# Kernel tuning notes

Measured on AMD Instinct MI355X. Metric: run time of the kernel, lower is better.

The kernel has to match this reference:

```python
import jax, jax.numpy as jnp
import numpy as np

B, C_IN, C_OUT, N = 4, 32, 32, 163842


def setup_inputs() -> dict:
    key = jax.random.key(0)
    k1, k2, k3, k4 = jax.random.split(key, 4)
    x = jax.random.normal(k1, (B, C_IN, N), dtype=jnp.float32)
    # nn.Linear(7*in_feats, out_feats): weight [out, 7*in], bias [out]
    W = jax.random.normal(k2, (C_OUT, 7 * C_IN), dtype=jnp.float32) * (1.0 / np.sqrt(7 * C_IN))
    b = jax.random.normal(k3, (C_OUT,), dtype=jnp.float32) * 0.01
    neigh_orders = jax.random.randint(k4, (N, 7), 0, N, dtype=jnp.int32)
    return {"x": x, "W": W, "b": b, "neigh_orders": neigh_orders}


def reference(x, W, b, neigh_orders):
    # x: [B, C_in, N] -> [B, N, C_in]
    xt = jnp.transpose(x, (0, 2, 1))
    # gather 1-ring neighborhood: [B, N, 7, C_in]
    gathered = xt[:, neigh_orders, :]
    Bb, Nn = xt.shape[0], xt.shape[1]
    mat = gathered.reshape(Bb, Nn, 7 * xt.shape[2])  # [B, N, 7*C_in]
    out = jnp.einsum("bnk,ok->bno", mat, W) + b       # [B, N, C_out]
    return jnp.transpose(out, (0, 2, 1))              # [B, C_out, N]
```

## Files before the change

### kernel.cpp

```cpp
#include <hip/hip_runtime.h>
#include <hip/hip_bf16.h>
#include <stdint.h>

#define B_   4
#define CIN  32
#define COUT 32
#define NV   163842
#define K7   7

typedef short bf16x8 __attribute__((ext_vector_type(8)));
typedef float f32x4  __attribute__((ext_vector_type(4)));

__device__ inline uint16_t f2bf(float f) {
    uint32_t u = __float_as_uint(f);
    uint32_t r = (u + 0x7FFFu + ((u >> 16) & 1u)) >> 16;
    return (uint16_t)r;
}

__global__ void k_convw(const float* __restrict__ W, uint16_t* __restrict__ Wb) {
    int i = blockIdx.x * 256 + threadIdx.x;
    if (i < COUT * K7 * CIN) Wb[i] = f2bf(W[i]);
}

__global__ void k_transpose(const float* __restrict__ x, uint16_t* __restrict__ xt) {
    int v = blockIdx.x * 256 + threadIdx.x;
    int b = blockIdx.y;
    if (v >= NV) return;
    const float* xb = x + (size_t)b * CIN * NV;
    uint16_t* row = xt + (size_t)v * (B_ * CIN) + b * CIN;
    #pragma unroll
    for (int q = 0; q < 4; ++q) {
        bf16x8 pk;
        #pragma unroll
        for (int i = 0; i < 8; ++i) {
            float f = xb[(size_t)(q * 8 + i) * NV + v];
            ((uint16_t*)&pk)[i] = f2bf(f);
        }
        *(bf16x8*)(row + q * 8) = pk;
    }
}

__global__ __launch_bounds__(256) void k_main(const uint16_t* __restrict__ xt,
                                              const uint16_t* __restrict__ Wb,
                                              const float* __restrict__ bias,
                                              const int* __restrict__ neigh,
                                              float* __restrict__ out) {
    const int tid  = threadIdx.x;
    const int lane = tid & 63;
    const int wv   = tid >> 6;
    const int vb   = blockIdx.x * 64 + wv * 16;
    const int l15  = lane & 15;
    const int g    = lane >> 4;
    const int v    = vb + l15;
    const int vv   = (v < NV) ? v : (NV - 1);

    bf16x8 wf[2][K7];
    #pragma unroll
    for (int t = 0; t < 2; ++t)
        #pragma unroll
        for (int j = 0; j < K7; ++j)
            wf[t][j] = *(const bf16x8*)(Wb + (size_t)(t * 16 + l15) * (K7 * CIN) + j * CIN + g * 8);

    int nidx[K7];
    #pragma unroll
    for (int j = 0; j < K7; ++j) nidx[j] = neigh[(size_t)vv * K7 + j];

    f32x4 acc[B_][2];
    #pragma unroll
    for (int b = 0; b < B_; ++b) {
        acc[b][0] = (f32x4){0.f, 0.f, 0.f, 0.f};
        acc[b][1] = (f32x4){0.f, 0.f, 0.f, 0.f};
    }

    #pragma unroll
    for (int j = 0; j < K7; ++j) {
        const uint16_t* row = xt + (size_t)nidx[j] * (B_ * CIN);
        bf16x8 xf[B_];
        #pragma unroll
        for (int b = 0; b < B_; ++b)
            xf[b] = *(const bf16x8*)(row + b * CIN + g * 8);
        #pragma unroll
        for (int b = 0; b < B_; ++b) {
            acc[b][0] = __builtin_amdgcn_mfma_f32_16x16x32_bf16(wf[0][j], xf[b], acc[b][0], 0, 0, 0);
            acc[b][1] = __builtin_amdgcn_mfma_f32_16x16x32_bf16(wf[1][j], xf[b], acc[b][1], 0, 0, 0);
        }
    }

    if (v < NV) {
        f32x4 bia0 = *(const f32x4*)(bias + g * 4);
        f32x4 bia1 = *(const f32x4*)(bias + 16 + g * 4);
        #pragma unroll
        for (int b = 0; b < B_; ++b) {
            float* ob = out + (size_t)b * COUT * NV + v;
            #pragma unroll
            for (int r = 0; r < 4; ++r) {
                int o0 = g * 4 + r;
                ob[(size_t)o0 * NV] = acc[b][0][r] + bia0[r];
                int o1 = 16 + g * 4 + r;
                ob[(size_t)o1 * NV] = acc[b][1][r] + bia1[r];
            }
        }
    }
}

extern "C" void kernel_launch(void* const* d_in, const int* in_sizes, int n_in,
                              void* d_out, int out_size, void* d_ws, size_t ws_size,
                              hipStream_t stream) {
    const float* x     = (const float*)d_in[0];
    const float* W     = (const float*)d_in[1];
    const float* bias  = (const float*)d_in[2];
    const int*   neigh = (const int*)d_in[3];
    float* out = (float*)d_out;

    uint16_t* xt = (uint16_t*)d_ws;
    uint16_t* Wb = xt + (size_t)NV * B_ * CIN;

    k_convw<<<(COUT * K7 * CIN + 255) / 256, 256, 0, stream>>>(W, Wb);

    dim3 g1((NV + 255) / 256, B_);
    k_transpose<<<g1, 256, 0, stream>>>(x, xt);

    dim3 g2((NV + 63) / 64, 1);
    k_main<<<g2, 256, 0, stream>>>(xt, Wb, bias, neigh, out);
}
```

Before: 244.2 us.

## Coalesce transpose stores via LDS and stage gathered rows through double-buffered LDS

The transpose kernel now packs 64 vertices across all batches into shared memory and then writes contiguous 16-byte chunks, so its global stores are coalesced instead of strided. The main kernel's gather is reorganised: each group of 4 lanes fetches one full 256-byte neighbour row with 16-byte loads. Those rows go into per-wave double-buffered LDS tiles with padding and are read back in MFMA operand layout, and the next neighbour's loads are issued early so they overlap with the current MFMAs. This costs extra LDS traffic and registers, and there is no explicit barrier between the intra-wave LDS writes and reads.

```diff
diff --git a/kernel.cpp b/kernel.cpp
--- a/kernel.cpp
+++ b/kernel.cpp
@@ -22,29 +22,50 @@
     if (i < COUT * K7 * CIN) Wb[i] = f2bf(W[i]);
 }
 
-__global__ void k_transpose(const float* __restrict__ x, uint16_t* __restrict__ xt) {
-    int v = blockIdx.x * 256 + threadIdx.x;
-    int b = blockIdx.y;
-    if (v >= NV) return;
-    const float* xb = x + (size_t)b * CIN * NV;
-    uint16_t* row = xt + (size_t)v * (B_ * CIN) + b * CIN;
+__global__ __launch_bounds__(256) void k_transpose(const float* __restrict__ x,
+                                                   uint16_t* __restrict__ xt) {
+    __shared__ uint16_t lds[64 * 132];
+    const int v0 = blockIdx.x * 64;
+    const int b  = threadIdx.x >> 6;
+    const int vl = threadIdx.x & 63;
+    const int v  = v0 + vl;
+
+    if (v < NV) {
+        const float* xb = x + (size_t)b * CIN * NV + v;
+        #pragma unroll
+        for (int q = 0; q < 4; ++q) {
+            bf16x8 pk;
+            #pragma unroll
+            for (int i = 0; i < 8; ++i)
+                ((uint16_t*)&pk)[i] = f2bf(xb[(size_t)(q * 8 + i) * NV]);
+            *(bf16x8*)&lds[vl * 132 + b * 32 + q * 8] = pk;
+        }
+    }
+    __syncthreads();
+
+    const size_t lim = ((size_t)(NV - v0)) * 256;
+    uint16_t* dst = xt + (size_t)v0 * 128;
+    const int tid = threadIdx.x;
     #pragma unroll
-    for (int q = 0; q < 4; ++q) {
-        bf16x8 pk;
-        #pragma unroll
-        for (int i = 0; i < 8; ++i) {
-            float f = xb[(size_t)(q * 8 + i) * NV + v];
-            ((uint16_t*)&pk)[i] = f2bf(f);
+    for (int s = 0; s < 4; ++s) {
+        const int f = s * 4096 + tid * 16;
+        if ((size_t)f < lim) {
+            const int row = f >> 8;
+            const int w   = f & 255;
+            bf16x8 d = *(bf16x8*)&lds[row * 132 + (w >> 1)];
+            *(bf16x8*)(dst + (f >> 1)) = d;
         }
-        *(bf16x8*)(row + q * 8) = pk;
     }
 }
+
+#define MFMA_BF16 __builtin_amdgcn_mfma_f32_16x16x32_bf16
 
 __global__ __launch_bounds__(256) void k_main(const uint16_t* __restrict__ xt,
                                               const uint16_t* __restrict__ Wb,
                                               const float* __restrict__ bias,
                                               const int* __restrict__ neigh,
                                               float* __restrict__ out) {
+    __shared__ uint16_t lds[4][2][16 * 132];
     const int tid  = threadIdx.x;
     const int lane = tid & 63;
     const int wv   = tid >> 6;
@@ -52,7 +73,10 @@
     const int l15  = lane & 15;
     const int g    = lane >> 4;
     const int v    = vb + l15;
-    const int vv   = (v < NV) ? v : (NV - 1);
+    const int gr   = lane >> 2;
+    const int gc   = lane & 3;
+    const int gv   = vb + gr;
+    const int gvv  = (gv < NV) ? gv : (NV - 1);
 
     bf16x8 wf[2][K7];
     #pragma unroll
@@ -61,9 +85,9 @@
         for (int j = 0; j < K7; ++j)
             wf[t][j] = *(const bf16x8*)(Wb + (size_t)(t * 16 + l15) * (K7 * CIN) + j * CIN + g * 8);
 
-    int nidx[K7];
+    int nidxg[K7];
     #pragma unroll
-    for (int j = 0; j < K7; ++j) nidx[j] = neigh[(size_t)vv * K7 + j];
+    for (int j = 0; j < K7; ++j) nidxg[j] = neigh[(size_t)gvv * K7 + j];
 
     f32x4 acc[B_][2];
     #pragma unroll
@@ -72,19 +96,42 @@
         acc[b][1] = (f32x4){0.f, 0.f, 0.f, 0.f};
     }
 
-    #pragma unroll
-    for (int j = 0; j < K7; ++j) {
-        const uint16_t* row = xt + (size_t)nidx[j] * (B_ * CIN);
-        bf16x8 xf[B_];
-        #pragma unroll
-        for (int b = 0; b < B_; ++b)
-            xf[b] = *(const bf16x8*)(row + b * CIN + g * 8);
-        #pragma unroll
-        for (int b = 0; b < B_; ++b) {
-            acc[b][0] = __builtin_amdgcn_mfma_f32_16x16x32_bf16(wf[0][j], xf[b], acc[b][0], 0, 0, 0);
-            acc[b][1] = __builtin_amdgcn_mfma_f32_16x16x32_bf16(wf[1][j], xf[b], acc[b][1], 0, 0, 0);
-        }
-    }
+    const char* xtb = (const char*)xt;
+    f32x4 ra0, ra1, ra2, ra3, rb0, rb1, rb2, rb3;
+
+#define ISSUE(R0, R1, R2, R3, j) { \
+    const char* _s = xtb + (size_t)nidxg[j] * 256 + gc * 16; \
+    R0 = *(const f32x4*)(_s);       R1 = *(const f32x4*)(_s + 64); \
+    R2 = *(const f32x4*)(_s + 128); R3 = *(const f32x4*)(_s + 192); }
+
+#define WRITE(R0, R1, R2, R3, BUF) { \
+    uint16_t* _d = &lds[wv][BUF][gr * 132 + gc * 8]; \
+    *(f32x4*)(_d)      = R0; *(f32x4*)(_d + 32) = R1; \
+    *(f32x4*)(_d + 64) = R2; *(f32x4*)(_d + 96) = R3; }
+
+#define RM(BUF, j) { \
+    const uint16_t* _r = &lds[wv][BUF][l15 * 132 + g * 8]; \
+    bf16x8 xf0 = *(const bf16x8*)(_r); \
+    bf16x8 xf1 = *(const bf16x8*)(_r + 32); \
+    bf16x8 xf2 = *(const bf16x8*)(_r + 64); \
+    bf16x8 xf3 = *(const bf16x8*)(_r + 96); \
+    acc[0][0] = MFMA_BF16(wf[0][j], xf0, acc[0][0], 0, 0, 0); \
+    acc[0][1] = MFMA_BF16(wf[1][j], xf0, acc[0][1], 0, 0, 0); \
+    acc[1][0] = MFMA_BF16(wf[0][j], xf1, acc[1][0], 0, 0, 0); \
+    acc[1][1] = MFMA_BF16(wf[1][j], xf1, acc[1][1], 0, 0, 0); \
+    acc[2][0] = MFMA_BF16(wf[0][j], xf2, acc[2][0], 0, 0, 0); \
+    acc[2][1] = MFMA_BF16(wf[1][j], xf2, acc[2][1], 0, 0, 0); \
+    acc[3][0] = MFMA_BF16(wf[0][j], xf3, acc[3][0], 0, 0, 0); \
+    acc[3][1] = MFMA_BF16(wf[1][j], xf3, acc[3][1], 0, 0, 0); }
+
+    ISSUE(ra0, ra1, ra2, ra3, 0);
+    ISSUE(rb0, rb1, rb2, rb3, 1); WRITE(ra0, ra1, ra2, ra3, 0); RM(0, 0);
+    ISSUE(ra0, ra1, ra2, ra3, 2); WRITE(rb0, rb1, rb2, rb3, 1); RM(1, 1);
+    ISSUE(rb0, rb1, rb2, rb3, 3); WRITE(ra0, ra1, ra2, ra3, 0); RM(0, 2);
+    ISSUE(ra0, ra1, ra2, ra3, 4); WRITE(rb0, rb1, rb2, rb3, 1); RM(1, 3);
+    ISSUE(rb0, rb1, rb2, rb3, 5); WRITE(ra0, ra1, ra2, ra3, 0); RM(0, 4);
+    ISSUE(ra0, ra1, ra2, ra3, 6); WRITE(rb0, rb1, rb2, rb3, 1); RM(1, 5);
+                                  WRITE(ra0, ra1, ra2, ra3, 0); RM(0, 6);
 
     if (v < NV) {
         f32x4 bia0 = *(const f32x4*)(bias + g * 4);
@@ -117,7 +164,7 @@
 
     k_convw<<<(COUT * K7 * CIN + 255) / 256, 256, 0, stream>>>(W, Wb);
 
-    dim3 g1((NV + 255) / 256, B_);
+    dim3 g1((NV + 63) / 64, 1);
     k_transpose<<<g1, 256, 0, stream>>>(x, xt);
 
     dim3 g2((NV + 63) / 64, 1);
```

Result: faster. 237.0 us (-2.9%).

## Stage transpose through LDS for coalesced writes and hoist all gathers in main

Applied to the files above, without the earlier changes.

The transpose kernel now handles 128 vertices across all batches per block, packs bf16 rows into padded shared memory, and writes the xt rows back as contiguous 16-byte chunks, so global stores are coalesced instead of strided by 256 bytes. In the main kernel, all 28 neighbor-row loads are issued before any MFMA, and launch bounds now request 2 blocks per CU, to get more memory-level parallelism. The cost is more registers held live for the prefetched fragments and 33 KB of LDS per transpose block.

```diff
diff --git a/kernel.cpp b/kernel.cpp
--- a/kernel.cpp
+++ b/kernel.cpp
@@ -22,29 +22,51 @@
     if (i < COUT * K7 * CIN) Wb[i] = f2bf(W[i]);
 }
 
-__global__ void k_transpose(const float* __restrict__ x, uint16_t* __restrict__ xt) {
-    int v = blockIdx.x * 256 + threadIdx.x;
-    int b = blockIdx.y;
-    if (v >= NV) return;
-    const float* xb = x + (size_t)b * CIN * NV;
-    uint16_t* row = xt + (size_t)v * (B_ * CIN) + b * CIN;
+__global__ __launch_bounds__(256) void k_transpose(const float* __restrict__ x,
+                                                   uint16_t* __restrict__ xt) {
+    __shared__ uint16_t lds[128 * 132];
+    const int v0 = blockIdx.x * 128;
+    const int t  = threadIdx.x;
+    const int vl = t & 127;
+    const int h  = t >> 7;
+    const int v  = v0 + vl;
+    const int vc = (v < NV) ? v : (NV - 1);
+
     #pragma unroll
-    for (int q = 0; q < 4; ++q) {
-        bf16x8 pk;
+    for (int b = 0; b < B_; ++b) {
+        const float* xb = x + (size_t)b * CIN * NV + (size_t)h * 16 * NV + vc;
         #pragma unroll
-        for (int i = 0; i < 8; ++i) {
-            float f = xb[(size_t)(q * 8 + i) * NV + v];
-            ((uint16_t*)&pk)[i] = f2bf(f);
+        for (int q = 0; q < 2; ++q) {
+            bf16x8 pk;
+            #pragma unroll
+            for (int i = 0; i < 8; ++i)
+                ((uint16_t*)&pk)[i] = f2bf(xb[(size_t)(q * 8 + i) * NV]);
+            *(bf16x8*)&lds[vl * 132 + b * 32 + h * 16 + q * 8] = pk;
         }
-        *(bf16x8*)(row + q * 8) = pk;
+    }
+    __syncthreads();
+
+    const size_t lim = ((size_t)(NV - v0)) * 256;
+    uint16_t* dst = xt + (size_t)v0 * 128;
+    #pragma unroll
+    for (int s = 0; s < 8; ++s) {
+        const int f = s * 4096 + t * 16;
+        if ((size_t)f < lim) {
+            const int row = f >> 8;
+            const int w   = f & 255;
+            bf16x8 d = *(bf16x8*)&lds[row * 132 + (w >> 1)];
+            *(bf16x8*)(dst + (f >> 1)) = d;
+        }
     }
 }
 
-__global__ __launch_bounds__(256) void k_main(const uint16_t* __restrict__ xt,
-                                              const uint16_t* __restrict__ Wb,
-                                              const float* __restrict__ bias,
-                                              const int* __restrict__ neigh,
-                                              float* __restrict__ out) {
+#define MFMA_BF16 __builtin_amdgcn_mfma_f32_16x16x32_bf16
+
+__global__ __launch_bounds__(256, 2) void k_main(const uint16_t* __restrict__ xt,
+                                                 const uint16_t* __restrict__ Wb,
+                                                 const float* __restrict__ bias,
+                                                 const int* __restrict__ neigh,
+                                                 float* __restrict__ out) {
     const int tid  = threadIdx.x;
     const int lane = tid & 63;
     const int wv   = tid >> 6;
@@ -54,16 +76,25 @@
     const int v    = vb + l15;
     const int vv   = (v < NV) ? v : (NV - 1);
 
+    int nidx[K7];
+    #pragma unroll
+    for (int j = 0; j < K7; ++j) nidx[j] = neigh[(size_t)vv * K7 + j];
+
+    bf16x8 xf[K7][B_];
+    #pragma unroll
+    for (int j = 0; j < K7; ++j) {
+        const uint16_t* row = xt + (size_t)nidx[j] * 128;
+        #pragma unroll
+        for (int b = 0; b < B_; ++b)
+            xf[j][b] = *(const bf16x8*)(row + b * 32 + g * 8);
+    }
+
     bf16x8 wf[2][K7];
     #pragma unroll
     for (int t = 0; t < 2; ++t)
         #pragma unroll
         for (int j = 0; j < K7; ++j)
             wf[t][j] = *(const bf16x8*)(Wb + (size_t)(t * 16 + l15) * (K7 * CIN) + j * CIN + g * 8);
-
-    int nidx[K7];
-    #pragma unroll
-    for (int j = 0; j < K7; ++j) nidx[j] = neigh[(size_t)vv * K7 + j];
 
     f32x4 acc[B_][2];
     #pragma unroll
@@ -73,18 +104,12 @@
     }
 
     #pragma unroll
-    for (int j = 0; j < K7; ++j) {
-        const uint16_t* row = xt + (size_t)nidx[j] * (B_ * CIN);
-        bf16x8 xf[B_];
-        #pragma unroll
-        for (int b = 0; b < B_; ++b)
-            xf[b] = *(const bf16x8*)(row + b * CIN + g * 8);
+    for (int j = 0; j < K7; ++j)
         #pragma unroll
         for (int b = 0; b < B_; ++b) {
-            acc[b][0] = __builtin_amdgcn_mfma_f32_16x16x32_bf16(wf[0][j], xf[b], acc[b][0], 0, 0, 0);
-            acc[b][1] = __builtin_amdgcn_mfma_f32_16x16x32_bf16(wf[1][j], xf[b], acc[b][1], 0, 0, 0);
+            acc[b][0] = MFMA_BF16(wf[0][j], xf[j][b], acc[b][0], 0, 0, 0);
+            acc[b][1] = MFMA_BF16(wf[1][j], xf[j][b], acc[b][1], 0, 0, 0);
         }
-    }
 
     if (v < NV) {
         f32x4 bia0 = *(const f32x4*)(bias + g * 4);
@@ -117,7 +142,7 @@
 
     k_convw<<<(COUT * K7 * CIN + 255) / 256, 256, 0, stream>>>(W, Wb);
 
-    dim3 g1((NV + 255) / 256, B_);
+    dim3 g1((NV + 127) / 128, 1);
     k_transpose<<<g1, 256, 0, stream>>>(x, xt);
 
     dim3 g2((NV + 63) / 64, 1);
```

Measured after the change: 239.5 us. About the same (-1.9%).
